# Performance work log

Measured on AMD Instinct MI355X. Metric: run time of the kernel, lower is better.

## Reference

```python
import jax, jax.numpy as jnp
import numpy as np

D_MODEL = 1024
NHEAD = 16
D_K = D_MODEL // NHEAD
B, S = 4, 2048
LN_EPS = 1e-5


def setup_inputs() -> dict:
    key = jax.random.key(0)
    ks = jax.random.split(key, 12)
    sd = 1.0 / np.sqrt(D_MODEL)
    inp = {
        'x': jax.random.normal(ks[0], (B, S, D_MODEL), dtype=jnp.float32),
        'wq': jax.random.normal(ks[1], (D_MODEL, D_MODEL), dtype=jnp.float32) * sd,
        'bq': jnp.zeros((D_MODEL,), dtype=jnp.float32),
        'wk': jax.random.normal(ks[2], (D_MODEL, D_MODEL), dtype=jnp.float32) * sd,
        'bk': jnp.zeros((D_MODEL,), dtype=jnp.float32),
        'wv': jax.random.normal(ks[3], (D_MODEL, D_MODEL), dtype=jnp.float32) * sd,
        'bv': jnp.zeros((D_MODEL,), dtype=jnp.float32),
        'wo': jax.random.normal(ks[4], (D_MODEL, D_MODEL), dtype=jnp.float32) * sd,
        'bo': jnp.zeros((D_MODEL,), dtype=jnp.float32),
        'conv_w': jax.random.normal(ks[5], (D_MODEL, 3), dtype=jnp.float32) * (1.0 / np.sqrt(3.0)),
        'conv_b': jnp.zeros((D_MODEL,), dtype=jnp.float32),
        'ln_g': jnp.ones((D_MODEL,), dtype=jnp.float32),
        'ln_b': jnp.zeros((D_MODEL,), dtype=jnp.float32),
    }
    return inp


def _forward(x, wq, bq, wk, bk, wv, bv, wo, bo, conv_w, conv_b, ln_g, ln_b):
    b, s, d = x.shape
    # QKV projections -> [B, H, S, Dk]
    q = (x @ wq.T + bq).reshape(b, s, NHEAD, D_K).transpose(0, 2, 1, 3)
    k = (x @ wk.T + bk).reshape(b, s, NHEAD, D_K).transpose(0, 2, 1, 3)
    v = (x @ wv.T + bv).reshape(b, s, NHEAD, D_K).transpose(0, 2, 1, 3)
    # full attention, materialized scores [B, H, S, S]
    scores = jnp.einsum('bhqd,bhkd->bhqk', q, k) / jnp.sqrt(jnp.float32(D_K))
    attn = jax.nn.softmax(scores, axis=-1)  # dropout is identity in eval
    ctx = jnp.einsum('bhqk,bhkd->bhqd', attn, v)
    ctx = ctx.transpose(0, 2, 1, 3).reshape(b, s, d)
    global_attn = ctx @ wo.T + bo
    # depthwise conv1d, kernel 3, padding 1 along sequence
    xp = jnp.pad(x, ((0, 0), (1, 1), (0, 0)))
    local_attn = (xp[:, :-2] * conv_w[:, 0]
                  + xp[:, 1:-1] * conv_w[:, 1]
                  + xp[:, 2:] * conv_w[:, 2]
                  + conv_b)
    combined = global_attn + 0.3 * local_attn
    y = x + combined  # dropout identity in eval
    mu = jnp.mean(y, axis=-1, keepdims=True)
    var = jnp.mean(jnp.square(y - mu), axis=-1, keepdims=True)
    return (y - mu) * jax.lax.rsqrt(var + LN_EPS) * ln_g + ln_b


def reference(x, wq, bq, wk, bk, wv, bv, wo, bo, conv_w, conv_b, ln_g, ln_b):
    return _forward(x, wq, bq, wk, bk, wv, bv, wo, bo, conv_w, conv_b, ln_g, ln_b)
```

## Files before the change

### kernel.cpp

```cpp
#include <hip/hip_runtime.h>

#define DEV __device__ __forceinline__

typedef unsigned short u16;
typedef unsigned int u32;
using f32x4  = __attribute__((ext_vector_type(4))) float;
using f32x16 = __attribute__((ext_vector_type(16))) float;
using s16x8  = __attribute__((ext_vector_type(8))) short;
using u32x2  = __attribute__((ext_vector_type(2))) u32;
using u32x4  = __attribute__((ext_vector_type(4))) u32;
typedef int i32x2 __attribute__((ext_vector_type(2)));

#if __has_builtin(__builtin_amdgcn_exp2f)
#define EXP2(x) __builtin_amdgcn_exp2f(x)
#else
#define EXP2(x) exp2f(x)
#endif

__constant__ const float C2_SCALE = 0.18033688011112042f;
#define S2_SHIFT 17.312340490667560f

DEV u16 f2b(float f) {
  union { float f; u32 u; } v; v.f = f;
  return (u16)((v.u + 0x7FFFu + ((v.u >> 16) & 1u)) >> 16);
}
DEV float b2f(u16 u) {
  union { u32 u; float f; } v; v.u = ((u32)u) << 16;
  return v.f;
}

DEV u32 cvtpk(float lo, float hi) {
  u32 r;
  asm("v_cvt_pk_bf16_f32 %0, %1, %2" : "=v"(r) : "v"(lo), "v"(hi));
  return r;
}

#if __has_builtin(__builtin_amdgcn_permlane32_swap)
DEV void lane32_swap(u32& x, u32& y) {
  i32x2 r = __builtin_amdgcn_permlane32_swap((int)x, (int)y, false, false);
  x = (u32)r[0]; y = (u32)r[1];
}
#else
DEV void lane32_swap(u32& x, u32& y) {
  u32 xo = (u32)__shfl_xor((int)x, 32, 64);
  u32 yo = (u32)__shfl_xor((int)y, 32, 64);
  int hi = (int)((threadIdx.x & 63) >> 5);
  u32 nx = hi ? yo : x;
  u32 ny = hi ? y : xo;
  x = nx; y = ny;
}
#endif

DEV void gload16(const void* g, void* l) {
  __builtin_amdgcn_global_load_lds(
      (const __attribute__((address_space(1))) void*)g,
      (__attribute__((address_space(3))) void*)l, 16, 0, 0);
}

__global__ __launch_bounds__(256) void k_cvt(const float* __restrict__ src,
                                             u16* __restrict__ dst, int n4) {
  int i = blockIdx.x * 256 + threadIdx.x;
  if (i >= n4) return;
  float4 v = ((const float4*)src)[i];
  ushort4 o;
  o.x = f2b(v.x); o.y = f2b(v.y); o.z = f2b(v.z); o.w = f2b(v.w);
  ((ushort4*)dst)[i] = o;
}

__global__ __launch_bounds__(256) void k_cvt_w(
    const float* __restrict__ s0, const float* __restrict__ s1,
    const float* __restrict__ s2, const float* __restrict__ s3,
    u16* __restrict__ dst) {
  int blk = blockIdx.x;
  int widx = blk >> 10;
  int i = (blk & 1023) * 256 + threadIdx.x;
  const float* src = widx == 0 ? s0 : widx == 1 ? s1 : widx == 2 ? s2 : s3;
  float4 v = ((const float4*)src)[i];
  ushort4 o;
  o.x = f2b(v.x); o.y = f2b(v.y); o.z = f2b(v.z); o.w = f2b(v.w);
  ((ushort4*)(dst + (size_t)widx * 1048576))[i] = o;
}

template <int MODE>
__global__ __launch_bounds__(256) void k_gemm_bt(
    const u16* __restrict__ A, const u16* __restrict__ Bw,
    const float* __restrict__ bias0, const float* __restrict__ bias1,
    u16* __restrict__ C, int M, int N, int K) {
  __shared__ alignas(16) u16 lds_[16384];
  char* lds = (char*)lds_;
  const int t = threadIdx.x;
  const int wave = t >> 6, lane = t & 63;
  const int g = lane >> 4, fr = lane & 15;
  const int wr = (wave >> 1) * 64, wc = (wave & 1) * 64;
  const int m0 = blockIdx.y * 128, n0 = blockIdx.x * 128;
  const int chunk = t & 3;

  auto stage = [&](int k0, int buf) {
#pragma unroll
    for (int r = 0; r < 2; ++r) {
      int row = r * 64 + (t >> 2);
      int sw = 8 * (chunk ^ ((row >> 1) & 3));
      char* dst = lds + buf * 16384 + r * 4096 + wave * 1024;
      gload16(A  + (size_t)(m0 + row) * K + k0 + sw, dst);
      gload16(Bw + (size_t)(n0 + row) * K + k0 + sw, dst + 8192);
    }
  };

  f32x4 acc[4][4];
#pragma unroll
  for (int i = 0; i < 4; ++i)
#pragma unroll
    for (int j = 0; j < 4; ++j)
#pragma unroll
      for (int r = 0; r < 4; ++r) acc[i][j][r] = 0.f;

  const int nk = K >> 5;
  stage(0, 0);
  __syncthreads();
  for (int kt = 0; kt < nk; ++kt) {
    const int cur = kt & 1;
    if (kt + 1 < nk) stage((kt + 1) << 5, cur ^ 1);
    s16x8 af[4], bf4[4];
#pragma unroll
    for (int i = 0; i < 4; ++i) {
      int row = wr + i * 16 + fr;
      af[i] = *(const s16x8*)(lds + cur * 16384 + row * 64 +
                              ((g * 16) ^ ((((row >> 1) & 3)) << 4)));
    }
#pragma unroll
    for (int j = 0; j < 4; ++j) {
      int row = wc + j * 16 + fr;
      bf4[j] = *(const s16x8*)(lds + cur * 16384 + 8192 + row * 64 +
                               ((g * 16) ^ ((((row >> 1) & 3)) << 4)));
    }
    __builtin_amdgcn_s_setprio(1);
#pragma unroll
    for (int i = 0; i < 4; ++i)
#pragma unroll
      for (int j = 0; j < 4; ++j)
        acc[i][j] = __builtin_amdgcn_mfma_f32_16x16x32_bf16(af[i], bf4[j], acc[i][j], 0, 0, 0);
    __builtin_amdgcn_s_setprio(0);
    __syncthreads();
  }
#pragma unroll
  for (int j = 0; j < 4; ++j) {
    const int coltile = n0 + wc + j * 16;
    float sc = 1.f;
    const float* bp = bias0;
    if constexpr (MODE == 2) {
      if (coltile >= 1024) { bp = bias1 - 1024; sc = C2_SCALE; }
    }
#pragma unroll
    for (int i = 0; i < 4; ++i)
#pragma unroll
      for (int r = 0; r < 4; ++r) {
        int row = m0 + wr + i * 16 + g * 4 + r;
        int col = coltile + fr;
        float v;
        if constexpr (MODE == 1) v = acc[i][j][r] + bias0[row];
        else                     v = (acc[i][j][r] + bp[col]) * sc;
        C[(size_t)row * N + col] = f2b(v);
      }
  }
}

__global__ __launch_bounds__(512, 4) void k_attn(
    const u16* __restrict__ qkb, const u16* __restrict__ vtb,
    u16* __restrict__ ctx) {
  __shared__ alignas(16) u16 smem_[16384];
  char* smem = (char*)smem_;
  const int bh = blockIdx.x;
  const int b = bh >> 4, h = bh & 15;
  const int qblk = blockIdx.y;
  const int t = threadIdx.x, w = t >> 6, lane = t & 63;
  const int l31 = lane & 31, hi = lane >> 5;
  const int hc = h * 64;
  const int q0 = qblk * 256 + w * 32;

  s16x8 qf[4];
  {
    const u16* qrow = qkb + (size_t)(b * 2048 + q0 + l31) * 2048 + hc + hi * 8;
#pragma unroll
    for (int ks = 0; ks < 4; ++ks) qf[ks] = *(const s16x8*)(qrow + ks * 16);
  }

  const u16* kbase  = qkb + (size_t)(b * 2048) * 2048 + 1024 + hc;
  const u16* vtbase = vtb + (size_t)hc * 8192 + b * 2048;

  const int srow = t >> 3, sseg = t & 7;
  const int ssw = 8 * (sseg ^ (srow & 7));
  auto stage = [&](int kt, int buf) {
    const int k0 = kt * 64;
    char* dst = smem + buf * 16384 + w * 1024;
    gload16(kbase  + (size_t)(k0 + srow) * 2048 + ssw, dst);
    gload16(vtbase + (size_t)srow * 8192 + k0 + ssw, dst + 8192);
  };

  f32x16 octx[2], lacc, ns2;
#pragma unroll
  for (int r = 0; r < 16; ++r) {
    octx[0][r] = 0.f; octx[1][r] = 0.f; lacc[r] = 0.f; ns2[r] = -S2_SHIFT;
  }
  s16x8 ones;
#pragma unroll
  for (int j = 0; j < 8; ++j) ones[j] = (short)0x3F80;

  stage(0, 0);
  __syncthreads();
  for (int kt = 0; kt < 32; ++kt) {
    const int cur = kt & 1;
    if (kt + 1 < 32) stage(kt + 1, cur ^ 1);

    f32x16 st[2];
    __builtin_amdgcn_s_setprio(1);
#pragma unroll
    for (int ks = 0; ks < 4; ++ks)
#pragma unroll
      for (int tt = 0; tt < 2; ++tt) {
        int row = tt * 32 + l31;
        s16x8 kf = *(const s16x8*)(smem + cur * 16384 + row * 128 +
                                   ((ks * 32 + hi * 16) ^ ((row & 7) << 4)));
        st[tt] = __builtin_amdgcn_mfma_f32_32x32x16_bf16(
            kf, qf[ks], ks == 0 ? ns2 : st[tt], 0, 0, 0);
      }
    __builtin_amdgcn_s_setprio(0);

    u32 pw[2][8];
#pragma unroll
    for (int tt = 0; tt < 2; ++tt)
#pragma unroll
      for (int p = 0; p < 8; ++p)
        pw[tt][p] = cvtpk(EXP2(st[tt][2 * p]), EXP2(st[tt][2 * p + 1]));

    s16x8 pf[4];
#pragma unroll
    for (int ks = 0; ks < 4; ++ks) {
      int tt = ks >> 1, kp = (ks & 1) * 4;
      u32 u0 = pw[tt][kp + 0], v0 = pw[tt][kp + 2];
      u32 u1 = pw[tt][kp + 1], v1 = pw[tt][kp + 3];
      lane32_swap(u0, v0);
      lane32_swap(u1, v1);
      u32x4 f; f[0] = u0; f[1] = u1; f[2] = v0; f[3] = v1;
      pf[ks] = __builtin_bit_cast(s16x8, f);
    }

    __builtin_amdgcn_s_setprio(1);
#pragma unroll
    for (int dt = 0; dt < 2; ++dt)
#pragma unroll
      for (int ks = 0; ks < 4; ++ks) {
        int row = dt * 32 + l31;
        s16x8 vf = *(const s16x8*)(smem + cur * 16384 + 8192 + row * 128 +
                                   ((ks * 32 + hi * 16) ^ ((row & 7) << 4)));
        octx[dt] = __builtin_amdgcn_mfma_f32_32x32x16_bf16(vf, pf[ks], octx[dt], 0, 0, 0);
      }
#pragma unroll
    for (int ks = 0; ks < 4; ++ks)
      lacc = __builtin_amdgcn_mfma_f32_32x32x16_bf16(ones, pf[ks], lacc, 0, 0, 0);
    __builtin_amdgcn_s_setprio(0);
    __syncthreads();
  }

  const float linv = 1.0f / lacc[0];

  const int ql = w * 32 + l31;
#pragma unroll
  for (int dt = 0; dt < 2; ++dt)
#pragma unroll
    for (int rq = 0; rq < 4; ++rq) {
      int d0 = 8 * rq + 4 * hi + 32 * dt;
      u32x2 pk;
      pk[0] = cvtpk(octx[dt][4 * rq + 0] * linv, octx[dt][4 * rq + 1] * linv);
      pk[1] = cvtpk(octx[dt][4 * rq + 2] * linv, octx[dt][4 * rq + 3] * linv);
      *(u32x2*)(smem + ql * 128 + ((2 * d0) ^ ((ql & 7) << 4))) = pk;
    }
  __syncthreads();
  {
    int qr = t >> 1, half = t & 1;
    u16* dst = ctx + (size_t)(b * 2048 + qblk * 256 + qr) * 1024 + hc + half * 32;
#pragma unroll
    for (int i = 0; i < 4; ++i) {
      s16x8 v = *(const s16x8*)(smem + qr * 128 +
                                ((half * 64 + i * 16) ^ ((qr & 7) << 4)));
      *(s16x8*)(dst + i * 8) = v;
    }
  }
}

__global__ __launch_bounds__(256) void k_epi(
    const float* __restrict__ x, const u16* __restrict__ gab,
    const float* __restrict__ cw, const float* __restrict__ cb,
    const float* __restrict__ lg, const float* __restrict__ lb,
    float* __restrict__ out) {
  __shared__ float red[4];
  const int n = blockIdx.x;
  const int s = n & 2047;
  const int t = threadIdx.x;
  const int d0 = t * 4;
  const float* xr = x + (size_t)n * 1024;

  float xc[4], xm[4], xp[4];
  { float4 v = *(const float4*)(xr + d0); xc[0]=v.x; xc[1]=v.y; xc[2]=v.z; xc[3]=v.w; }
  if (s > 0) { float4 v = *(const float4*)(xr - 1024 + d0); xm[0]=v.x; xm[1]=v.y; xm[2]=v.z; xm[3]=v.w; }
  else { xm[0]=xm[1]=xm[2]=xm[3]=0.f; }
  if (s < 2047) { float4 v = *(const float4*)(xr + 1024 + d0); xp[0]=v.x; xp[1]=v.y; xp[2]=v.z; xp[3]=v.w; }
  else { xp[0]=xp[1]=xp[2]=xp[3]=0.f; }
  ushort4 gv = *(const ushort4*)(gab + (size_t)n * 1024 + d0);
  float ga4[4] = { b2f(gv.x), b2f(gv.y), b2f(gv.z), b2f(gv.w) };

  float y[4];
#pragma unroll
  for (int i = 0; i < 4; ++i) {
    int d = d0 + i;
    float lo = xm[i] * cw[d * 3] + xc[i] * cw[d * 3 + 1] + xp[i] * cw[d * 3 + 2] + cb[d];
    y[i] = xc[i] + ga4[i] + 0.3f * lo;
  }

  float sm = y[0] + y[1] + y[2] + y[3];
#pragma unroll
  for (int off = 32; off >= 1; off >>= 1) sm += __shfl_xor(sm, off, 64);
  if ((t & 63) == 0) red[t >> 6] = sm;
  __syncthreads();
  float mu = (red[0] + red[1] + red[2] + red[3]) * (1.f / 1024.f);
  __syncthreads();

  float vs = 0.f;
#pragma unroll
  for (int i = 0; i < 4; ++i) { float dd = y[i] - mu; vs += dd * dd; }
#pragma unroll
  for (int off = 32; off >= 1; off >>= 1) vs += __shfl_xor(vs, off, 64);
  if ((t & 63) == 0) red[t >> 6] = vs;
  __syncthreads();
  float var = (red[0] + red[1] + red[2] + red[3]) * (1.f / 1024.f);
  float rs = rsqrtf(var + 1e-5f);
#pragma unroll
  for (int i = 0; i < 4; ++i) {
    int d = d0 + i;
    out[(size_t)n * 1024 + d] = (y[i] - mu) * rs * lg[d] + lb[d];
  }
}

extern "C" void kernel_launch(void* const* d_in, const int* in_sizes, int n_in,
                              void* d_out, int out_size, void* d_ws, size_t ws_size,
                              hipStream_t stream) {
  const float* x  = (const float*)d_in[0];
  const float* wq = (const float*)d_in[1];
  const float* bq = (const float*)d_in[2];
  const float* wk = (const float*)d_in[3];
  const float* bk = (const float*)d_in[4];
  const float* wv = (const float*)d_in[5];
  const float* bv = (const float*)d_in[6];
  const float* wo = (const float*)d_in[7];
  const float* bo = (const float*)d_in[8];
  const float* cw = (const float*)d_in[9];
  const float* cb = (const float*)d_in[10];
  const float* lg = (const float*)d_in[11];
  const float* lb = (const float*)d_in[12];
  float* out = (float*)d_out;

  char* ws = (char*)d_ws;
  const size_t MB = 1ull << 20;
  u16* xb  = (u16*)(ws + 0);
  u16* wqb = (u16*)(ws + 16 * MB);
  u16* wkb = (u16*)(ws + 18 * MB);
  u16* wvb = (u16*)(ws + 20 * MB);
  u16* wob = (u16*)(ws + 22 * MB);
  u16* qkb = (u16*)(ws + 24 * MB);
  u16* vtb = (u16*)(ws + 56 * MB);
  u16* ctx = xb;
  u16* gab = qkb;

  k_cvt<<<8192, 256, 0, stream>>>(x, xb, 2097152);
  k_cvt_w<<<4096, 256, 0, stream>>>(wq, wk, wv, wo, wqb);

  k_gemm_bt<2><<<dim3(16, 64), 256, 0, stream>>>(xb, wqb, bq, bk, qkb, 8192, 2048, 1024);
  k_gemm_bt<1><<<dim3(64, 8), 256, 0, stream>>>(wvb, xb, bv, nullptr, vtb, 1024, 8192, 1024);

  k_attn<<<dim3(64, 8), 512, 0, stream>>>(qkb, vtb, ctx);

  k_gemm_bt<0><<<dim3(8, 64), 256, 0, stream>>>(ctx, wob, bo, nullptr, gab, 8192, 1024, 1024);

  k_epi<<<8192, 256, 0, stream>>>(x, gab, cw, cb, lg, lb, out);
}
```

Baseline: 219.0 us.

## Triple-buffer LDS staging with explicit vmcnt waits in GEMM and attention

Both the projection GEMM and the attention kernel move from double to triple-buffered global-to-LDS staging. Loads are issued two tiles ahead, and partial s_waitcnt vmcnt waits replace full __syncthreads, so more memory latency overlaps with MFMA work. In exchange LDS per block grows by half, which may cut occupancy: attention goes to 48KB per block with a launch-bounds target of 4 blocks. The waits now rely on hand-counted outstanding loads, which is fragile if the compiler reorders instructions.

```diff
diff --git a/kernel.cpp b/kernel.cpp
--- a/kernel.cpp
+++ b/kernel.cpp
@@ -16,6 +16,8 @@
 #else
 #define EXP2(x) exp2f(x)
 #endif
+
+#define WAITV(N) asm volatile("s_waitcnt vmcnt(" #N ")" ::: "memory")
 
 __constant__ const float C2_SCALE = 0.18033688011112042f;
 #define S2_SHIFT 17.312340490667560f
@@ -86,7 +88,7 @@
     const u16* __restrict__ A, const u16* __restrict__ Bw,
     const float* __restrict__ bias0, const float* __restrict__ bias1,
     u16* __restrict__ C, int M, int N, int K) {
-  __shared__ alignas(16) u16 lds_[16384];
+  __shared__ alignas(16) u16 lds_[24576];
   char* lds = (char*)lds_;
   const int t = threadIdx.x;
   const int wave = t >> 6, lane = t & 63;
@@ -95,7 +97,8 @@
   const int m0 = blockIdx.y * 128, n0 = blockIdx.x * 128;
   const int chunk = t & 3;
 
-  auto stage = [&](int k0, int buf) {
+  auto stage = [&](int kt, int buf) {
+    const int k0 = kt << 5;
 #pragma unroll
     for (int r = 0; r < 2; ++r) {
       int row = r * 64 + (t >> 2);
@@ -116,10 +119,15 @@
 
   const int nk = K >> 5;
   stage(0, 0);
-  __syncthreads();
+  stage(1, 1);
+  int cur = 0;
   for (int kt = 0; kt < nk; ++kt) {
-    const int cur = kt & 1;
-    if (kt + 1 < nk) stage((kt + 1) << 5, cur ^ 1);
+    int nslot = cur + 2; if (nslot >= 3) nslot -= 3;
+    if (kt + 2 < nk) { stage(kt + 2, nslot); WAITV(8); }
+    else if (kt + 1 < nk) WAITV(4);
+    else WAITV(0);
+    __builtin_amdgcn_s_barrier();
+    __builtin_amdgcn_sched_barrier(0);
     s16x8 af[4], bf4[4];
 #pragma unroll
     for (int i = 0; i < 4; ++i) {
@@ -140,7 +148,9 @@
       for (int j = 0; j < 4; ++j)
         acc[i][j] = __builtin_amdgcn_mfma_f32_16x16x32_bf16(af[i], bf4[j], acc[i][j], 0, 0, 0);
     __builtin_amdgcn_s_setprio(0);
-    __syncthreads();
+    __builtin_amdgcn_sched_barrier(0);
+    __builtin_amdgcn_s_barrier();
+    cur = cur + 1; if (cur >= 3) cur -= 3;
   }
 #pragma unroll
   for (int j = 0; j < 4; ++j) {
@@ -167,7 +177,7 @@
 __global__ __launch_bounds__(512, 4) void k_attn(
     const u16* __restrict__ qkb, const u16* __restrict__ vtb,
     u16* __restrict__ ctx) {
-  __shared__ alignas(16) u16 smem_[16384];
+  __shared__ alignas(16) u16 smem_[24576];
   char* smem = (char*)smem_;
   const int bh = blockIdx.x;
   const int b = bh >> 4, h = bh & 15;
@@ -183,6 +193,7 @@
 #pragma unroll
     for (int ks = 0; ks < 4; ++ks) qf[ks] = *(const s16x8*)(qrow + ks * 16);
   }
+  WAITV(0);
 
   const u16* kbase  = qkb + (size_t)(b * 2048) * 2048 + 1024 + hc;
   const u16* vtbase = vtb + (size_t)hc * 8192 + b * 2048;
@@ -206,10 +217,15 @@
   for (int j = 0; j < 8; ++j) ones[j] = (short)0x3F80;
 
   stage(0, 0);
-  __syncthreads();
+  stage(1, 1);
+  int cur = 0;
   for (int kt = 0; kt < 32; ++kt) {
-    const int cur = kt & 1;
-    if (kt + 1 < 32) stage(kt + 1, cur ^ 1);
+    int nslot = cur + 2; if (nslot >= 3) nslot -= 3;
+    if (kt + 2 < 32) { stage(kt + 2, nslot); WAITV(4); }
+    else if (kt + 1 < 32) WAITV(2);
+    else WAITV(0);
+    __builtin_amdgcn_s_barrier();
+    __builtin_amdgcn_sched_barrier(0);
 
     f32x16 st[2];
     __builtin_amdgcn_s_setprio(1);
@@ -258,7 +274,9 @@
     for (int ks = 0; ks < 4; ++ks)
       lacc = __builtin_amdgcn_mfma_f32_32x32x16_bf16(ones, pf[ks], lacc, 0, 0, 0);
     __builtin_amdgcn_s_setprio(0);
-    __syncthreads();
+    __builtin_amdgcn_sched_barrier(0);
+    __builtin_amdgcn_s_barrier();
+    cur = cur + 1; if (cur >= 3) cur -= 3;
   }
 
   const float linv = 1.0f / lacc[0];
```

Measured after the change: 220.0 us. No clear change (+0.5%).

## Process two query sub-tiles per wave in attention and sum row-sums in registers

Applied to the files above, without the earlier changes.

The attention kernel now runs 256 threads per block, and each wave handles 64 query rows as two 32-row sub-tiles. Each K/V fragment read from shared memory is reused across both sub-tiles, which halves LDS reads per MFMA. The softmax denominator is now accumulated from the exp values in registers with a cross-half lane swap, replacing the extra MFMA against a ones vector. The cost is higher register pressure, since accumulators double, and fewer waves per block to hide latency.

```diff
diff --git a/kernel.cpp b/kernel.cpp
--- a/kernel.cpp
+++ b/kernel.cpp
@@ -164,7 +164,7 @@
   }
 }
 
-__global__ __launch_bounds__(512, 4) void k_attn(
+__global__ __launch_bounds__(256, 2) void k_attn(
     const u16* __restrict__ qkb, const u16* __restrict__ vtb,
     u16* __restrict__ ctx) {
   __shared__ alignas(16) u16 smem_[16384];
@@ -175,35 +175,40 @@
   const int t = threadIdx.x, w = t >> 6, lane = t & 63;
   const int l31 = lane & 31, hi = lane >> 5;
   const int hc = h * 64;
-  const int q0 = qblk * 256 + w * 32;
-
-  s16x8 qf[4];
-  {
-    const u16* qrow = qkb + (size_t)(b * 2048 + q0 + l31) * 2048 + hc + hi * 8;
-#pragma unroll
-    for (int ks = 0; ks < 4; ++ks) qf[ks] = *(const s16x8*)(qrow + ks * 16);
+  const int q0 = qblk * 256 + w * 64;
+
+  s16x8 qf[2][4];
+#pragma unroll
+  for (int s = 0; s < 2; ++s) {
+    const u16* qrow = qkb + (size_t)(b * 2048 + q0 + s * 32 + l31) * 2048 + hc + hi * 8;
+#pragma unroll
+    for (int ks = 0; ks < 4; ++ks) qf[s][ks] = *(const s16x8*)(qrow + ks * 16);
   }
 
   const u16* kbase  = qkb + (size_t)(b * 2048) * 2048 + 1024 + hc;
   const u16* vtbase = vtb + (size_t)hc * 8192 + b * 2048;
 
-  const int srow = t >> 3, sseg = t & 7;
-  const int ssw = 8 * (sseg ^ (srow & 7));
+  const int lrow = lane >> 3, seg = lane & 7;
   auto stage = [&](int kt, int buf) {
     const int k0 = kt * 64;
-    char* dst = smem + buf * 16384 + w * 1024;
-    gload16(kbase  + (size_t)(k0 + srow) * 2048 + ssw, dst);
-    gload16(vtbase + (size_t)srow * 8192 + k0 + ssw, dst + 8192);
+#pragma unroll
+    for (int r = 0; r < 2; ++r) {
+      int row = r * 32 + w * 8 + lrow;
+      int sw = 8 * (seg ^ (row & 7));
+      char* dst = smem + buf * 16384 + r * 4096 + w * 1024;
+      gload16(kbase  + (size_t)(k0 + row) * 2048 + sw, dst);
+      gload16(vtbase + (size_t)row * 8192 + k0 + sw, dst + 8192);
+    }
   };
 
-  f32x16 octx[2], lacc, ns2;
+  f32x16 octx[2][2], ns2;
 #pragma unroll
   for (int r = 0; r < 16; ++r) {
-    octx[0][r] = 0.f; octx[1][r] = 0.f; lacc[r] = 0.f; ns2[r] = -S2_SHIFT;
-  }
-  s16x8 ones;
-#pragma unroll
-  for (int j = 0; j < 8; ++j) ones[j] = (short)0x3F80;
+    octx[0][0][r] = 0.f; octx[0][1][r] = 0.f;
+    octx[1][0][r] = 0.f; octx[1][1][r] = 0.f;
+    ns2[r] = -S2_SHIFT;
+  }
+  float lrun[2] = {0.f, 0.f};
 
   stage(0, 0);
   __syncthreads();
@@ -211,37 +216,46 @@
     const int cur = kt & 1;
     if (kt + 1 < 32) stage(kt + 1, cur ^ 1);
 
-    f32x16 st[2];
-    __builtin_amdgcn_s_setprio(1);
-#pragma unroll
-    for (int ks = 0; ks < 4; ++ks)
-#pragma unroll
-      for (int tt = 0; tt < 2; ++tt) {
-        int row = tt * 32 + l31;
-        s16x8 kf = *(const s16x8*)(smem + cur * 16384 + row * 128 +
-                                   ((ks * 32 + hi * 16) ^ ((row & 7) << 4)));
-        st[tt] = __builtin_amdgcn_mfma_f32_32x32x16_bf16(
-            kf, qf[ks], ks == 0 ? ns2 : st[tt], 0, 0, 0);
+    s16x8 pf[2][4];
+#pragma unroll
+    for (int s = 0; s < 2; ++s) {
+      f32x16 st[2];
+      __builtin_amdgcn_s_setprio(1);
+#pragma unroll
+      for (int ks = 0; ks < 4; ++ks)
+#pragma unroll
+        for (int tt = 0; tt < 2; ++tt) {
+          int row = tt * 32 + l31;
+          s16x8 kf = *(const s16x8*)(smem + cur * 16384 + row * 128 +
+                                     ((ks * 32 + hi * 16) ^ ((row & 7) << 4)));
+          st[tt] = __builtin_amdgcn_mfma_f32_32x32x16_bf16(
+              kf, qf[s][ks], ks == 0 ? ns2 : st[tt], 0, 0, 0);
+        }
+      __builtin_amdgcn_s_setprio(0);
+
+      u32 pw[2][8];
+      float sm = 0.f;
+#pragma unroll
+      for (int tt = 0; tt < 2; ++tt)
+#pragma unroll
+        for (int p = 0; p < 8; ++p) {
+          float plo = EXP2(st[tt][2 * p]);
+          float phi = EXP2(st[tt][2 * p + 1]);
+          sm += plo + phi;
+          pw[tt][p] = cvtpk(plo, phi);
+        }
+      lrun[s] += sm;
+
+#pragma unroll
+      for (int ks = 0; ks < 4; ++ks) {
+        int tt = ks >> 1, kp = (ks & 1) * 4;
+        u32 u0 = pw[tt][kp + 0], v0 = pw[tt][kp + 2];
+        u32 u1 = pw[tt][kp + 1], v1 = pw[tt][kp + 3];
+        lane32_swap(u0, v0);
+        lane32_swap(u1, v1);
+        u32x4 f; f[0] = u0; f[1] = u1; f[2] = v0; f[3] = v1;
+        pf[s][ks] = __builtin_bit_cast(s16x8, f);
       }
-    __builtin_amdgcn_s_setprio(0);
-
-    u32 pw[2][8];
-#pragma unroll
-    for (int tt = 0; tt < 2; ++tt)
-#pragma unroll
-      for (int p = 0; p < 8; ++p)
-        pw[tt][p] = cvtpk(EXP2(st[tt][2 * p]), EXP2(st[tt][2 * p + 1]));
-
-    s16x8 pf[4];
-#pragma unroll
-    for (int ks = 0; ks < 4; ++ks) {
-      int tt = ks >> 1, kp = (ks & 1) * 4;
-      u32 u0 = pw[tt][kp + 0], v0 = pw[tt][kp + 2];
-      u32 u1 = pw[tt][kp + 1], v1 = pw[tt][kp + 3];
-      lane32_swap(u0, v0);
-      lane32_swap(u1, v1);
-      u32x4 f; f[0] = u0; f[1] = u1; f[2] = v0; f[3] = v1;
-      pf[ks] = __builtin_bit_cast(s16x8, f);
     }
 
     __builtin_amdgcn_s_setprio(1);
@@ -252,36 +266,42 @@
         int row = dt * 32 + l31;
         s16x8 vf = *(const s16x8*)(smem + cur * 16384 + 8192 + row * 128 +
                                    ((ks * 32 + hi * 16) ^ ((row & 7) << 4)));
-        octx[dt] = __builtin_amdgcn_mfma_f32_32x32x16_bf16(vf, pf[ks], octx[dt], 0, 0, 0);
+        octx[0][dt] = __builtin_amdgcn_mfma_f32_32x32x16_bf16(vf, pf[0][ks], octx[0][dt], 0, 0, 0);
+        octx[1][dt] = __builtin_amdgcn_mfma_f32_32x32x16_bf16(vf, pf[1][ks], octx[1][dt], 0, 0, 0);
       }
-#pragma unroll
-    for (int ks = 0; ks < 4; ++ks)
-      lacc = __builtin_amdgcn_mfma_f32_32x32x16_bf16(ones, pf[ks], lacc, 0, 0, 0);
     __builtin_amdgcn_s_setprio(0);
     __syncthreads();
   }
 
-  const float linv = 1.0f / lacc[0];
-
-  const int ql = w * 32 + l31;
-#pragma unroll
-  for (int dt = 0; dt < 2; ++dt)
-#pragma unroll
-    for (int rq = 0; rq < 4; ++rq) {
-      int d0 = 8 * rq + 4 * hi + 32 * dt;
-      u32x2 pk;
-      pk[0] = cvtpk(octx[dt][4 * rq + 0] * linv, octx[dt][4 * rq + 1] * linv);
-      pk[1] = cvtpk(octx[dt][4 * rq + 2] * linv, octx[dt][4 * rq + 3] * linv);
-      *(u32x2*)(smem + ql * 128 + ((2 * d0) ^ ((ql & 7) << 4))) = pk;
-    }
+  float linv[2];
+#pragma unroll
+  for (int s = 0; s < 2; ++s) {
+    u32 ua = __builtin_bit_cast(u32, lrun[s]), va = ua;
+    lane32_swap(ua, va);
+    linv[s] = 1.0f / (__builtin_bit_cast(float, ua) + __builtin_bit_cast(float, va));
+  }
+
+#pragma unroll
+  for (int s = 0; s < 2; ++s) {
+    const int ql = w * 64 + s * 32 + l31;
+#pragma unroll
+    for (int dt = 0; dt < 2; ++dt)
+#pragma unroll
+      for (int rq = 0; rq < 4; ++rq) {
+        int d0 = 8 * rq + 4 * hi + 32 * dt;
+        u32x2 pk;
+        pk[0] = cvtpk(octx[s][dt][4 * rq + 0] * linv[s], octx[s][dt][4 * rq + 1] * linv[s]);
+        pk[1] = cvtpk(octx[s][dt][4 * rq + 2] * linv[s], octx[s][dt][4 * rq + 3] * linv[s]);
+        *(u32x2*)(smem + ql * 128 + ((2 * d0) ^ ((ql & 7) << 4))) = pk;
+      }
+  }
   __syncthreads();
   {
-    int qr = t >> 1, half = t & 1;
-    u16* dst = ctx + (size_t)(b * 2048 + qblk * 256 + qr) * 1024 + hc + half * 32;
-#pragma unroll
-    for (int i = 0; i < 4; ++i) {
-      s16x8 v = *(const s16x8*)(smem + qr * 128 +
-                                ((half * 64 + i * 16) ^ ((qr & 7) << 4)));
+    int qr = t;
+    u16* dst = ctx + (size_t)(b * 2048 + qblk * 256 + qr) * 1024 + hc;
+#pragma unroll
+    for (int i = 0; i < 8; ++i) {
+      s16x8 v = *(const s16x8*)(smem + qr * 128 + ((i * 16) ^ ((qr & 7) << 4)));
       *(s16x8*)(dst + i * 8) = v;
     }
   }
@@ -376,7 +396,7 @@
   k_gemm_bt<2><<<dim3(16, 64), 256, 0, stream>>>(xb, wqb, bq, bk, qkb, 8192, 2048, 1024);
   k_gemm_bt<1><<<dim3(64, 8), 256, 0, stream>>>(wvb, xb, bv, nullptr, vtb, 1024, 8192, 1024);
 
-  k_attn<<<dim3(64, 8), 512, 0, stream>>>(qkb, vtb, ctx);
+  k_attn<<<dim3(64, 8), 256, 0, stream>>>(qkb, vtb, ctx);
 
   k_gemm_bt<0><<<dim3(8, 64), 256, 0, stream>>>(ctx, wob, bo, nullptr, gab, 8192, 1024, 1024);
 
```

Result: faster. 207.7 us (-5.1%).
